# Kernel tuning notes

Hardware: AMD Instinct MI355X
Metric: run time of the kernel (lower is better)

Reference implementation:

```python
import jax, jax.numpy as jnp
import numpy as np

KERNEL_SIZE = 3
FILTERS = 512


def setup_inputs() -> dict:
    key = jax.random.key(0)
    k1, k2 = jax.random.split(key)
    B, T, D, K, F = 8, 2048, 512, KERNEL_SIZE, FILTERS
    x = jax.random.normal(k1, (B, T, D), dtype=jnp.float32)
    kernels = jax.random.normal(k2, (B, T, K, F), dtype=jnp.float32)
    return {"x": x, "kernels": kernels}


def reference(x, kernels):
    # x: [B, T, D], kernels: [B, T, K, F] -> out: [B, T, F]
    B, T, D = x.shape
    K = kernels.shape[2]
    pad = K // 2
    xp = jnp.pad(x, ((0, 0), (pad, pad), (0, 0)))  # [B, T+2*pad, D]
    # Sliding windows along T: patches[b, t, k, d] = xp[b, t + k, d]
    patches = jnp.stack([xp[:, k:k + T, :] for k in range(K)], axis=2)  # [B, T, K, D]
    # Faithful to tf.einsum('btkd,btkf->btf'): sums over BOTH k and d.
    out = jnp.einsum('btkd,btkf->btf', patches, kernels)
    return out
```

## Files before the change

kernel.cpp:

```cpp
#include <hip/hip_runtime.h>


#define B_ 8
#define T_ 2048
#define D_ 512
#define F_ 512
#define TCHUNK 16
#define CHUNKS_PER_B (T_ / TCHUNK)

__global__ __launch_bounds__(256) void fused_conv(
    const float* __restrict__ x, const float* __restrict__ kern,
    float* __restrict__ out) {
    __shared__ float Ssh[TCHUNK + 2];

    const int chunk = blockIdx.x;
    const int b  = chunk / CHUNKS_PER_B;
    const int t0 = (chunk - b * CHUNKS_PER_B) * TCHUNK;
    const int wave = threadIdx.x >> 6;
    const int lane = threadIdx.x & 63;

    for (int r = wave; r < TCHUNK + 2; r += 4) {
        const int t = t0 - 1 + r;
        float s = 0.0f;
        if (t >= 0 && t < T_) {
            const float4* xr = (const float4*)(x + ((size_t)b * T_ + t) * D_);
            float4 a = xr[lane];
            float4 c = xr[lane + 64];
            s = (a.x + a.y) + (a.z + a.w) + (c.x + c.y) + (c.z + c.w);
            #pragma unroll
            for (int off = 32; off > 0; off >>= 1)
                s += __shfl_down(s, off, 64);
        }
        if (lane == 0) Ssh[r] = s;
    }
    __syncthreads();

    const int fi   = threadIdx.x & 127;
    const int rsub = threadIdx.x >> 7;
    #pragma unroll
    for (int r = rsub; r < TCHUNK; r += 2) {
        const size_t bt = (size_t)b * T_ + t0 + r;
        const float4* kr = (const float4*)(kern + bt * (size_t)(3 * F_));
        const float s0 = Ssh[r];
        const float s1 = Ssh[r + 1];
        const float s2 = Ssh[r + 2];
        float4 k0 = kr[fi];
        float4 k1 = kr[fi + (F_ / 4)];
        float4 k2 = kr[fi + 2 * (F_ / 4)];
        float4 o;
        o.x = s0 * k0.x + s1 * k1.x + s2 * k2.x;
        o.y = s0 * k0.y + s1 * k1.y + s2 * k2.y;
        o.z = s0 * k0.z + s1 * k1.z + s2 * k2.z;
        o.w = s0 * k0.w + s1 * k1.w + s2 * k2.w;
        ((float4*)(out + bt * F_))[fi] = o;
    }
}

extern "C" void kernel_launch(void* const* d_in, const int* in_sizes, int n_in,
                              void* d_out, int out_size, void* d_ws, size_t ws_size,
                              hipStream_t stream) {
    const float* x    = (const float*)d_in[0];
    const float* kern = (const float*)d_in[1];
    float* out = (float*)d_out;
    (void)d_ws; (void)ws_size;

    fused_conv<<<(B_ * T_) / TCHUNK, 256, 0, stream>>>(x, kern, out);
}
```

Measured before the change: 180.7 us.

## Make each wave independently handle two timesteps, issuing all loads up front

```diff
diff --git a/kernel.cpp b/kernel.cpp
--- a/kernel.cpp
+++ b/kernel.cpp
@@ -5,54 +5,68 @@
 #define T_ 2048
 #define D_ 512
 #define F_ 512
-#define TCHUNK 16
-#define CHUNKS_PER_B (T_ / TCHUNK)
 
-__global__ __launch_bounds__(256) void fused_conv(
+__global__ __launch_bounds__(256, 4) void fused_wave(
     const float* __restrict__ x, const float* __restrict__ kern,
     float* __restrict__ out) {
-    __shared__ float Ssh[TCHUNK + 2];
+    const int wid  = (blockIdx.x << 2) + (threadIdx.x >> 6);
+    const int lane = threadIdx.x & 63;
+    const int b  = wid >> 10;
+    const int t0 = (wid & 1023) << 1;
+    const size_t bt0 = (size_t)b * T_ + t0;
 
-    const int chunk = blockIdx.x;
-    const int b  = chunk / CHUNKS_PER_B;
-    const int t0 = (chunk - b * CHUNKS_PER_B) * TCHUNK;
-    const int wave = threadIdx.x >> 6;
-    const int lane = threadIdx.x & 63;
+    float4 xa[4][2];
+    #pragma unroll
+    for (int j = 0; j < 4; ++j) {
+        const int u = t0 - 1 + j;
+        if (u >= 0 && u < T_) {
+            const float4* xr = (const float4*)(x + ((size_t)b * T_ + u) * D_);
+            xa[j][0] = xr[lane];
+            xa[j][1] = xr[lane + 64];
+        } else {
+            xa[j][0] = make_float4(0.f, 0.f, 0.f, 0.f);
+            xa[j][1] = make_float4(0.f, 0.f, 0.f, 0.f);
+        }
+    }
 
-    for (int r = wave; r < TCHUNK + 2; r += 4) {
-        const int t = t0 - 1 + r;
-        float s = 0.0f;
-        if (t >= 0 && t < T_) {
-            const float4* xr = (const float4*)(x + ((size_t)b * T_ + t) * D_);
-            float4 a = xr[lane];
-            float4 c = xr[lane + 64];
-            s = (a.x + a.y) + (a.z + a.w) + (c.x + c.y) + (c.z + c.w);
-            #pragma unroll
-            for (int off = 32; off > 0; off >>= 1)
-                s += __shfl_down(s, off, 64);
+    float4 kk[2][3][2];
+    #pragma unroll
+    for (int r = 0; r < 2; ++r) {
+        const float4* kr = (const float4*)(kern + (bt0 + r) * (size_t)(3 * F_));
+        #pragma unroll
+        for (int k = 0; k < 3; ++k) {
+            kk[r][k][0] = kr[k * (F_ / 4) + lane];
+            kk[r][k][1] = kr[k * (F_ / 4) + lane + 64];
         }
-        if (lane == 0) Ssh[r] = s;
     }
-    __syncthreads();
 
-    const int fi   = threadIdx.x & 127;
-    const int rsub = threadIdx.x >> 7;
+    float S[4];
     #pragma unroll
-    for (int r = rsub; r < TCHUNK; r += 2) {
-        const size_t bt = (size_t)b * T_ + t0 + r;
-        const float4* kr = (const float4*)(kern + bt * (size_t)(3 * F_));
-        const float s0 = Ssh[r];
-        const float s1 = Ssh[r + 1];
-        const float s2 = Ssh[r + 2];
-        float4 k0 = kr[fi];
-        float4 k1 = kr[fi + (F_ / 4)];
-        float4 k2 = kr[fi + 2 * (F_ / 4)];
-        float4 o;
-        o.x = s0 * k0.x + s1 * k1.x + s2 * k2.x;
-        o.y = s0 * k0.y + s1 * k1.y + s2 * k2.y;
-        o.z = s0 * k0.z + s1 * k1.z + s2 * k2.z;
-        o.w = s0 * k0.w + s1 * k1.w + s2 * k2.w;
-        ((float4*)(out + bt * F_))[fi] = o;
+    for (int j = 0; j < 4; ++j) {
+        const float4 a = xa[j][0], c = xa[j][1];
+        float s = (a.x + a.y) + (a.z + a.w) + (c.x + c.y) + (c.z + c.w);
+        #pragma unroll
+        for (int off = 32; off > 0; off >>= 1)
+            s += __shfl_xor(s, off, 64);
+        S[j] = s;
+    }
+
+    #pragma unroll
+    for (int r = 0; r < 2; ++r) {
+        float4* orow = (float4*)(out + (bt0 + r) * F_);
+        const float s0 = S[r], s1 = S[r + 1], s2 = S[r + 2];
+        #pragma unroll
+        for (int h = 0; h < 2; ++h) {
+            const float4 k0 = kk[r][0][h];
+            const float4 k1 = kk[r][1][h];
+            const float4 k2 = kk[r][2][h];
+            float4 o;
+            o.x = s0 * k0.x + s1 * k1.x + s2 * k2.x;
+            o.y = s0 * k0.y + s1 * k1.y + s2 * k2.y;
+            o.z = s0 * k0.z + s1 * k1.z + s2 * k2.z;
+            o.w = s0 * k0.w + s1 * k1.w + s2 * k2.w;
+            orow[lane + 64 * h] = o;
+        }
     }
 }
 
@@ -64,5 +78,5 @@
     float* out = (float*)d_out;
     (void)d_ws; (void)ws_size;
 
-    fused_conv<<<(B_ * T_) / TCHUNK, 256, 0, stream>>>(x, kern, out);
+    fused_wave<<<(B_ * T_) / 8, 256, 0, stream>>>(x, kern, out);
 }
```

Measured after the change: 178.5 us. About the same (-1.2%).
